# Performance work log

Hardware: AMD Instinct MI355X
Metric: run time of the kernel (lower is better)

Reference implementation:

```python
import jax, jax.numpy as jnp
import numpy as np
import math

HID_DIM = 1024
NUM_HEADS = 8
QK_DIM = HID_DIM // 8  # 128 total, 16 per head


def setup_inputs() -> dict:
    key = jax.random.key(0)
    ks = jax.random.split(key, 7)
    B, M, C = 4, 2048, HID_DIM
    gain = math.sqrt(2.0)  # calculate_gain('relu')

    def xavier(k, fan_in, fan_out):
        std = gain * math.sqrt(2.0 / (fan_in + fan_out))
        a = math.sqrt(3.0) * std
        return jax.random.uniform(k, (fan_out, fan_in), jnp.float32, -a, a)

    x = jax.random.normal(ks[0], (B, M, C), jnp.float32)
    Wq = xavier(ks[1], C, QK_DIM)   # [out, in] like torch Linear
    Wk = xavier(ks[2], C, QK_DIM)
    Wv = xavier(ks[3], C, C)
    bq = jnp.zeros((QK_DIM,), jnp.float32)
    bk = jnp.zeros((QK_DIM,), jnp.float32)
    bv = jnp.zeros((C,), jnp.float32)
    gamma = jnp.zeros((1,), jnp.float32)
    return {"x": x, "Wq": Wq, "bq": bq, "Wk": Wk, "bk": bk,
            "Wv": Wv, "bv": bv, "gamma": gamma}


def reference(x, Wq, bq, Wk, bk, Wv, bv, gamma):
    B, M, C = x.shape
    H = NUM_HEADS
    dqk = QK_DIM // H   # per-head qk dim = 16
    dv = C // H         # per-head v dim = 128
    q = (x @ Wq.T + bq).reshape(B, M, H, dqk)  # [B,M,H,dqk]
    k = (x @ Wk.T + bk).reshape(B, M, H, dqk)
    v = (x @ Wv.T + bv).reshape(B, M, H, dv)
    scores = jnp.einsum('bmhd,bnhd->bhmn', q, k) / math.sqrt(dqk)
    scores = jnp.where(scores >= 0, scores, 0.2 * scores)  # LeakyReLU(0.2)
    beta = jax.nn.softmax(scores, axis=-1)                 # [B,H,M,M]
    out = jnp.einsum('bhmn,bnhd->bmhd', beta, v).reshape(B, M, C)
    return gamma * out + x
```

## Files before the change

### kernel.cpp

```cpp
#include <hip/hip_runtime.h>
#include <hip/hip_bf16.h>

typedef __bf16 bf16_t;
typedef __bf16 bf16x8 __attribute__((ext_vector_type(8)));
typedef float f32x4 __attribute__((ext_vector_type(4)));
typedef float f32x16 __attribute__((ext_vector_type(16)));

#define MTOT 8192
#define CDIM 1024
#define HEADS 8
#define DV 128
#define QKD 128
#define SEQ 2048
#define QSCALE 0.3606737602222409f

struct alignas(8) B4 { bf16_t a, b, c, d; };

__device__ inline bf16x8 cvt8(float4 a, float4 b) {
    bf16x8 v = { (bf16_t)a.x, (bf16_t)a.y, (bf16_t)a.z, (bf16_t)a.w,
                 (bf16_t)b.x, (bf16_t)b.y, (bf16_t)b.z, (bf16_t)b.w };
    return v;
}

__device__ inline void gl_lds16(const bf16_t* g, bf16_t* l) {
    __builtin_amdgcn_global_load_lds(
        (const __attribute__((address_space(1))) void*)g,
        (__attribute__((address_space(3))) void*)l, 16, 0, 0);
}

__device__ inline unsigned cvtpk(float a, float b) {
    unsigned r;
    asm("v_cvt_pk_bf16_f32 %0, %1, %2" : "=v"(r) : "v"(a), "v"(b));
    return r;
}

__device__ inline void plswap(unsigned& a, unsigned& b) {
    asm("v_permlane32_swap_b32 %0, %1" : "+v"(a), "+v"(b));
}

#define XITEMS (MTOT * CDIM / 8)
#define WITEMS (1280 * CDIM / 8)

__global__ __launch_bounds__(256) void cvt_all(
    const float* __restrict__ X,
    const float* __restrict__ Wq, const float* __restrict__ Wk,
    const float* __restrict__ Wv,
    bf16_t* __restrict__ Xb, bf16_t* __restrict__ Wb)
{
    int i = blockIdx.x * blockDim.x + threadIdx.x;
    if (i < XITEMS) {
        const float4* s = reinterpret_cast<const float4*>(X) + (size_t)i * 2;
        reinterpret_cast<bf16x8*>(Xb)[i] = cvt8(s[0], s[1]);
    } else {
        int j = i - XITEMS;
        const float* src;
        if (j < 16384)       src = Wq + (size_t)j * 8;
        else if (j < 32768)  src = Wk + (size_t)(j - 16384) * 8;
        else                 src = Wv + (size_t)(j - 32768) * 8;
        const float4* s = reinterpret_cast<const float4*>(src);
        reinterpret_cast<bf16x8*>(Wb)[j] = cvt8(s[0], s[1]);
    }
}

__global__ __launch_bounds__(256) void qkv_gemm3(
    const bf16_t* __restrict__ Xb, const bf16_t* __restrict__ Wb,
    const float* __restrict__ bq, const float* __restrict__ bk,
    const float* __restrict__ bv,
    bf16_t* __restrict__ Qw, bf16_t* __restrict__ Kw, bf16_t* __restrict__ Vt)
{
    __shared__ bf16_t As[128][64];
    __shared__ bf16_t Bs[128][64];

    const int tid = threadIdx.x;
    const int w = tid >> 6, l = tid & 63;
    const int c = l & 15, q = l >> 4;
    const int rw = w & 1, cw = w >> 1;
    const int bx = blockIdx.x;
    const int m0 = blockIdx.y * 128;

    const bf16_t* Arow = Xb + (size_t)(m0 + w * 8 + (l >> 3)) * CDIM + (l & 7) * 8;
    const bf16_t* Brow = Wb + (size_t)(bx * 128 + w * 8 + (l >> 3)) * CDIM + (l & 7) * 8;

    f32x4 acc[16] = {};

    for (int k0 = 0; k0 < CDIM; k0 += 64) {
        __syncthreads();
        #pragma unroll
        for (int i = 0; i < 4; ++i) {
            gl_lds16(Arow + k0 + (size_t)i * 32 * CDIM, &As[i * 32 + w * 8][0]);
            gl_lds16(Brow + k0 + (size_t)i * 32 * CDIM, &Bs[i * 32 + w * 8][0]);
        }
        __syncthreads();
        #pragma unroll
        for (int kk = 0; kk < 2; ++kk) {
            bf16x8 af[4], bfr[4];
            #pragma unroll
            for (int mt = 0; mt < 4; ++mt)
                af[mt] = *(const bf16x8*)&As[rw * 64 + mt * 16 + c][kk * 32 + q * 8];
            #pragma unroll
            for (int nt = 0; nt < 4; ++nt)
                bfr[nt] = *(const bf16x8*)&Bs[cw * 64 + nt * 16 + c][kk * 32 + q * 8];
            #pragma unroll
            for (int mt = 0; mt < 4; ++mt)
                #pragma unroll
                for (int nt = 0; nt < 4; ++nt)
                    acc[mt * 4 + nt] = __builtin_amdgcn_mfma_f32_16x16x32_bf16(
                        af[mt], bfr[nt], acc[mt * 4 + nt], 0, 0, 0);
        }
    }

    #pragma unroll
    for (int mt = 0; mt < 4; ++mt)
        #pragma unroll
        for (int nt = 0; nt < 4; ++nt) {
            const int cl = cw * 64 + nt * 16 + c;
            f32x4 a = acc[mt * 4 + nt];
            const int mg = m0 + rw * 64 + mt * 16 + q * 4;
            if (bx == 0) {
                const float bb = bq[cl];
                #pragma unroll
                for (int r = 0; r < 4; ++r)
                    Qw[(size_t)(mg + r) * QKD + cl] = (bf16_t)((a[r] + bb) * QSCALE);
            } else if (bx == 1) {
                const float bb = bk[cl];
                #pragma unroll
                for (int r = 0; r < 4; ++r)
                    Kw[(size_t)(mg + r) * QKD + cl] = (bf16_t)(a[r] + bb);
            } else {
                const int h = bx - 2;
                const float bb = bv[h * DV + cl];
                const int bidx = mg >> 11, ml = mg & 2047;
                B4 v{ (bf16_t)(a[0] + bb), (bf16_t)(a[1] + bb),
                      (bf16_t)(a[2] + bb), (bf16_t)(a[3] + bb) };
                *(B4*)(Vt + ((size_t)(bidx * HEADS + h) * DV + cl) * SEQ + ml) = v;
            }
        }
}

__global__ __launch_bounds__(256, 2) void qkv_gemm2(
    const float* __restrict__ X,
    const float* __restrict__ Wq, const float* __restrict__ bq,
    const float* __restrict__ Wk, const float* __restrict__ bk,
    const float* __restrict__ Wv, const float* __restrict__ bv,
    bf16_t* __restrict__ Qw, bf16_t* __restrict__ Kw, bf16_t* __restrict__ Vt)
{
    __shared__ alignas(16) bf16_t As[128][72];
    __shared__ alignas(16) bf16_t Bs[128][72];

    const int tid  = threadIdx.x;
    const int lane = tid & 63, wave = tid >> 6;
    const int c = lane & 15, q = lane >> 4;
    const int rw = wave & 1, cw = wave >> 1;
    const int m0 = blockIdx.y * 128;
    const int nt_idx = blockIdx.x;

    const float* W; const float* bias;
    if (nt_idx == 0)      { W = Wq; bias = bq; }
    else if (nt_idx == 1) { W = Wk; bias = bk; }
    else { W = Wv + (size_t)(nt_idx - 2) * DV * CDIM; bias = bv + (nt_idx - 2) * DV; }

    const int srow = tid >> 1, sseg = tid & 1;
    const int swr = (srow >> 3) & 3;
    const float* ax = X + (size_t)(m0 + srow) * CDIM + sseg * 32;
    const float* bxp = W + (size_t)srow * CDIM + sseg * 32;

    f32x4 acc[16] = {};

    for (int k0 = 0; k0 < CDIM; k0 += 64) {
        __syncthreads();
        #pragma unroll
        for (int i = 0; i < 4; ++i) {
            const int ph = (sseg * 4 + i) ^ swr;
            *(bf16x8*)&As[srow][ph * 8] = cvt8(*(const float4*)(ax + k0 + i * 8),
                                               *(const float4*)(ax + k0 + i * 8 + 4));
            *(bf16x8*)&Bs[srow][ph * 8] = cvt8(*(const float4*)(bxp + k0 + i * 8),
                                               *(const float4*)(bxp + k0 + i * 8 + 4));
        }
        __syncthreads();
        #pragma unroll
        for (int kk = 0; kk < 2; ++kk) {
            bf16x8 af[4], bfr[4];
            #pragma unroll
            for (int mt = 0; mt < 4; ++mt) {
                const int row = rw * 64 + mt * 16 + c;
                af[mt] = *(const bf16x8*)&As[row][((kk * 4 + q) ^ ((row >> 3) & 3)) * 8];
            }
            #pragma unroll
            for (int nt = 0; nt < 4; ++nt) {
                const int row = cw * 64 + nt * 16 + c;
                bfr[nt] = *(const bf16x8*)&Bs[row][((kk * 4 + q) ^ ((row >> 3) & 3)) * 8];
            }
            #pragma unroll
            for (int mt = 0; mt < 4; ++mt)
                #pragma unroll
                for (int nt = 0; nt < 4; ++nt)
                    acc[mt * 4 + nt] = __builtin_amdgcn_mfma_f32_16x16x32_bf16(
                        af[mt], bfr[nt], acc[mt * 4 + nt], 0, 0, 0);
        }
    }

    #pragma unroll
    for (int mt = 0; mt < 4; ++mt)
        #pragma unroll
        for (int nt = 0; nt < 4; ++nt) {
            const int col = cw * 64 + nt * 16 + c;
            const float bb = bias[col];
            f32x4 a = acc[mt * 4 + nt];
            const int mg = m0 + rw * 64 + mt * 16 + q * 4;
            if (nt_idx == 0) {
                #pragma unroll
                for (int r = 0; r < 4; ++r)
                    Qw[(size_t)(mg + r) * QKD + col] = (bf16_t)((a[r] + bb) * QSCALE);
            } else if (nt_idx == 1) {
                #pragma unroll
                for (int r = 0; r < 4; ++r)
                    Kw[(size_t)(mg + r) * QKD + col] = (bf16_t)(a[r] + bb);
            } else {
                const int h = nt_idx - 2;
                const int bidx = mg >> 11, ml = mg & 2047;
                B4 v{ (bf16_t)(a[0] + bb), (bf16_t)(a[1] + bb),
                      (bf16_t)(a[2] + bb), (bf16_t)(a[3] + bb) };
                *(B4*)(Vt + ((size_t)(bidx * HEADS + h) * DV + col) * SEQ + ml) = v;
            }
        }
}

__global__ __launch_bounds__(256, 2) void attn3(
    const bf16_t* __restrict__ Q, const bf16_t* __restrict__ K,
    const bf16_t* __restrict__ Vt, const float* __restrict__ X,
    const float* __restrict__ gptr, float* __restrict__ out)
{
    __shared__ alignas(16) bf16_t Vs[2][128][68];

    const int tid  = threadIdx.x;
    const int lane = tid & 63;
    const int c5 = lane & 31, q1 = lane >> 5;

    const int lin = blockIdx.x + (SEQ / 128) * blockIdx.y;
    const int xcd = lin & 7, jj = lin >> 3;
    const int bh = xcd * 4 + (jj >> 4);
    const int qt = jj & 15;
    const int b = bh >> 3, h = bh & 7;
    const int wave = tid >> 6;
    const int mbase = qt * 128 + wave * 32;

    const bf16x8 qf = *(const bf16x8*)(
        Q + (size_t)(b * SEQ + mbase + c5) * QKD + h * 16 + q1 * 8);

    const bf16x8 ones = { (bf16_t)1.0f, (bf16_t)1.0f, (bf16_t)1.0f, (bf16_t)1.0f,
                          (bf16_t)1.0f, (bf16_t)1.0f, (bf16_t)1.0f, (bf16_t)1.0f };

    f32x16 o[4] = {};
    f32x16 oli = {};

    const bf16_t* Vhead = Vt + (size_t)(b * HEADS + h) * DV * SEQ;
    const bf16_t* Kbase = K + (size_t)(b * SEQ) * QKD + h * 16;

    const int sdv = tid >> 1, sseg = tid & 1;
    const int swv = (sdv >> 3) & 7;

    bf16x8 vA[4], vB[4], kA[2], kB[2];

    union U8 { bf16x8 v; unsigned u[4]; unsigned long long q[2]; };

    #define VS_WR(buf, row, ph, val) do {                                    \
        U8 _u; _u.v = (val);                                                 \
        *(unsigned long long*)&Vs[buf][row][(ph) * 8]     = _u.q[0];         \
        *(unsigned long long*)&Vs[buf][row][(ph) * 8 + 4] = _u.q[1];         \
    } while (0)

    {
        const bf16_t* s0 = Vhead + (size_t)sdv * SEQ + sseg * 32;
        #pragma unroll
        for (int i = 0; i < 4; ++i) vA[i] = *(const bf16x8*)(s0 + i * 8);
        const bf16_t* s1 = s0 + 64;
        #pragma unroll
        for (int i = 0; i < 4; ++i) vB[i] = *(const bf16x8*)(s1 + i * 8);
        #pragma unroll
        for (int blk = 0; blk < 2; ++blk) {
            kA[blk] = *(const bf16x8*)(Kbase + (size_t)(blk * 32 + c5) * QKD + q1 * 8);
            kB[blk] = *(const bf16x8*)(Kbase + (size_t)(64 + blk * 32 + c5) * QKD + q1 * 8);
        }
        #pragma unroll
        for (int i = 0; i < 4; ++i) {
            const int ph = (sseg * 4 + i) ^ swv;
            VS_WR(0, sdv, ph, vA[i]);
        }
        const bf16_t* s2 = s0 + 128;
        #pragma unroll
        for (int i = 0; i < 4; ++i) vA[i] = *(const bf16x8*)(s2 + i * 8);
    }

    #pragma unroll 1
    for (int t = 0; t < 32; t += 2) {
        #pragma unroll
        for (int half = 0; half < 2; ++half) {
            asm volatile("s_waitcnt lgkmcnt(0)" ::: "memory");
            __builtin_amdgcn_s_barrier();
            __builtin_amdgcn_sched_barrier(0);

            #pragma unroll
            for (int i = 0; i < 4; ++i) {
                const int ph = (sseg * 4 + i) ^ swv;
                if (half) { VS_WR(0, sdv, ph, vA[i]); }
                else      { VS_WR(1, sdv, ph, vB[i]); }
            }
            const int cur = t + half;
            const bf16x8 k0f = half ? kB[0] : kA[0];
            const bf16x8 k1f = half ? kB[1] : kA[1];
            {
                const int vt  = (cur + 3 < 32) ? cur + 3 : 31;
                const int kt2 = (cur + 2 < 32) ? cur + 2 : 31;
                const bf16_t* src = Vhead + (size_t)sdv * SEQ + vt * 64 + sseg * 32;
                #pragma unroll
                for (int i = 0; i < 4; ++i) {
                    bf16x8 vv = *(const bf16x8*)(src + i * 8);
                    if (half) vA[i] = vv; else vB[i] = vv;
                }
                #pragma unroll
                for (int blk = 0; blk < 2; ++blk) {
                    bf16x8 kk = *(const bf16x8*)(
                        Kbase + (size_t)(kt2 * 64 + blk * 32 + c5) * QKD + q1 * 8);
                    if (half) kB[blk] = kk; else kA[blk] = kk;
                }
            }

            U8 frag[4];
            #pragma unroll
            for (int blk = 0; blk < 2; ++blk) {
                f32x16 z = {};
                f32x16 s = __builtin_amdgcn_mfma_f32_32x32x16_bf16(
                    blk ? k1f : k0f, qf, z, 0, 0, 0);
                float e[16];
                #pragma unroll
                for (int r = 0; r < 16; ++r) {
                    const float sv = s[r];
                    e[r] = __builtin_amdgcn_exp2f(fmaxf(sv, 0.2f * sv));
                }
                unsigned w0 = cvtpk(e[0], e[1]),   w1 = cvtpk(e[2], e[3]);
                unsigned w2 = cvtpk(e[4], e[5]),   w3 = cvtpk(e[6], e[7]);
                unsigned w4 = cvtpk(e[8], e[9]),   w5 = cvtpk(e[10], e[11]);
                unsigned w6 = cvtpk(e[12], e[13]), w7 = cvtpk(e[14], e[15]);
                plswap(w0, w2); plswap(w1, w3);
                plswap(w4, w6); plswap(w5, w7);
                frag[blk * 2 + 0].u[0] = w0; frag[blk * 2 + 0].u[1] = w1;
                frag[blk * 2 + 0].u[2] = w2; frag[blk * 2 + 0].u[3] = w3;
                frag[blk * 2 + 1].u[0] = w4; frag[blk * 2 + 1].u[1] = w5;
                frag[blk * 2 + 1].u[2] = w6; frag[blk * 2 + 1].u[3] = w7;
            }

            __builtin_amdgcn_s_setprio(1);
            #pragma unroll
            for (int kt = 0; kt < 4; ++kt) {
                const bf16x8 pa = frag[kt].v;
                #pragma unroll
                for (int dvt = 0; dvt < 4; ++dvt) {
                    const int dv = dvt * 32 + c5;
                    const int phB = (kt * 2 + q1) ^ ((dv >> 3) & 7);
                    U8 ur;
                    ur.q[0] = *(const unsigned long long*)&Vs[half][dv][phB * 8];
                    ur.q[1] = *(const unsigned long long*)&Vs[half][dv][phB * 8 + 4];
                    o[dvt] = __builtin_amdgcn_mfma_f32_32x32x16_bf16(
                        pa, ur.v, o[dvt], 0, 0, 0);
                }
                oli = __builtin_amdgcn_mfma_f32_32x32x16_bf16(pa, ones, oli, 0, 0, 0);
            }
            __builtin_amdgcn_s_setprio(0);
        }
    }

    const float g = gptr[0];

    #pragma unroll
    for (int r = 0; r < 16; ++r) {
        const int row = (r & 3) + 8 * (r >> 2) + 4 * q1;
        const float inv = 1.f / oli[r];
        #pragma unroll
        for (int dvt = 0; dvt < 4; ++dvt) {
            const size_t idx = (size_t)(b * SEQ + mbase + row) * CDIM
                             + h * DV + dvt * 32 + c5;
            out[idx] = g * (o[dvt][r] * inv) + X[idx];
        }
    }
    #undef VS_WR
}

extern "C" void kernel_launch(void* const* d_in, const int* in_sizes, int n_in,
                              void* d_out, int out_size, void* d_ws, size_t ws_size,
                              hipStream_t stream) {
    const float* X  = (const float*)d_in[0];
    const float* Wq = (const float*)d_in[1];
    const float* bq = (const float*)d_in[2];
    const float* Wk = (const float*)d_in[3];
    const float* bk = (const float*)d_in[4];
    const float* Wv = (const float*)d_in[5];
    const float* bv = (const float*)d_in[6];
    const float* g  = (const float*)d_in[7];
    float* out = (float*)d_out;

    dim3 blk(256);
    const size_t big_elems = (size_t)MTOT * CDIM + 1280 * CDIM
                           + (size_t)MTOT * QKD * 2 + (size_t)MTOT * CDIM;
    const size_t big_ws = big_elems * sizeof(bf16_t);

    if (ws_size >= big_ws) {
        bf16_t* Xb = (bf16_t*)d_ws;
        bf16_t* Wb = Xb + (size_t)MTOT * CDIM;
        bf16_t* Qw = Wb + (size_t)1280 * CDIM;
        bf16_t* Kw = Qw + (size_t)MTOT * QKD;
        bf16_t* Vt = Kw + (size_t)MTOT * QKD;

        hipLaunchKernelGGL(cvt_all, dim3((XITEMS + WITEMS) / 256), blk, 0, stream,
                           X, Wq, Wk, Wv, Xb, Wb);
        hipLaunchKernelGGL(qkv_gemm3, dim3(10, 64), blk, 0, stream,
                           Xb, Wb, bq, bk, bv, Qw, Kw, Vt);
        hipLaunchKernelGGL(attn3, dim3(SEQ / 128, 32), blk, 0, stream,
                           Qw, Kw, Vt, X, g, out);
    } else {
        bf16_t* Qw = (bf16_t*)d_ws;
        bf16_t* Kw = Qw + (size_t)MTOT * QKD;
        bf16_t* Vt = Kw + (size_t)MTOT * QKD;
        hipLaunchKernelGGL(qkv_gemm2, dim3(10, 64), blk, 0, stream,
                           X, Wq, bq, Wk, bk, Wv, bv, Qw, Kw, Vt);
        hipLaunchKernelGGL(attn3, dim3(SEQ / 128, 32), blk, 0, stream,
                           Qw, Kw, Vt, X, g, out);
    }
}
```

Baseline: 209.9 us.

## Software-pipeline QK softmax one tile ahead and replace ones-MFMA row sum with VALU

Restructures the attention inner loop so the QK^T scores and exp for tile t+1 are computed while the PV MFMAs for tile t run. This lets VALU exp work overlap matrix-core work instead of serializing with it. The softmax denominator, previously computed with an extra MFMA against a ones vector, is now accumulated with scalar adds per lane and combined with a cross-lane shuffle at the end. This costs more live registers for the double fragment buffers and sums the denominator from fp32 values rather than the bf16-rounded ones.

```diff
diff --git a/kernel.cpp b/kernel.cpp
--- a/kernel.cpp
+++ b/kernel.cpp
@@ -15,6 +15,7 @@
 #define QSCALE 0.3606737602222409f
 
 struct alignas(8) B4 { bf16_t a, b, c, d; };
+union U8 { bf16x8 v; unsigned u[4]; unsigned long long q[2]; };
 
 __device__ inline bf16x8 cvt8(float4 a, float4 b) {
     bf16x8 v = { (bf16_t)a.x, (bf16_t)a.y, (bf16_t)a.z, (bf16_t)a.w,
@@ -247,11 +248,8 @@
     const bf16x8 qf = *(const bf16x8*)(
         Q + (size_t)(b * SEQ + mbase + c5) * QKD + h * 16 + q1 * 8);
 
-    const bf16x8 ones = { (bf16_t)1.0f, (bf16_t)1.0f, (bf16_t)1.0f, (bf16_t)1.0f,
-                          (bf16_t)1.0f, (bf16_t)1.0f, (bf16_t)1.0f, (bf16_t)1.0f };
-
+    float li = 0.f;
     f32x16 o[4] = {};
-    f32x16 oli = {};
 
     const bf16_t* Vhead = Vt + (size_t)(b * HEADS + h) * DV * SEQ;
     const bf16_t* Kbase = K + (size_t)(b * SEQ) * QKD + h * 16;
@@ -260,8 +258,7 @@
     const int swv = (sdv >> 3) & 7;
 
     bf16x8 vA[4], vB[4], kA[2], kB[2];
-
-    union U8 { bf16x8 v; unsigned u[4]; unsigned long long q[2]; };
+    U8 fragE[4], fragO[4];
 
     #define VS_WR(buf, row, ph, val) do {                                    \
         U8 _u; _u.v = (val);                                                 \
@@ -269,6 +266,70 @@
         *(unsigned long long*)&Vs[buf][row][(ph) * 8 + 4] = _u.q[1];         \
     } while (0)
 
+    #define QKSM(KF0, KF1, FR) do {                                          \
+        f32x16 _z = {};                                                      \
+        f32x16 _sa = __builtin_amdgcn_mfma_f32_32x32x16_bf16(KF0, qf, _z, 0, 0, 0); \
+        f32x16 _sb = __builtin_amdgcn_mfma_f32_32x32x16_bf16(KF1, qf, _z, 0, 0, 0); \
+        float _ea[16], _eb[16];                                              \
+        _Pragma("unroll")                                                    \
+        for (int _r = 0; _r < 16; ++_r) {                                    \
+            const float _v = _sa[_r];                                        \
+            _ea[_r] = __builtin_amdgcn_exp2f(fmaxf(_v, 0.2f * _v));          \
+            const float _w = _sb[_r];                                        \
+            _eb[_r] = __builtin_amdgcn_exp2f(fmaxf(_w, 0.2f * _w));          \
+        }                                                                    \
+        {                                              \
+            const float _q0 = (_ea[0] + _ea[1]) + (_ea[2] + _ea[3]);         \
+            const float _q1 = (_ea[4] + _ea[5]) + (_ea[6] + _ea[7]);         \
+            const float _q2 = (_ea[8] + _ea[9]) + (_ea[10] + _ea[11]);       \
+            const float _q3 = (_ea[12] + _ea[13]) + (_ea[14] + _ea[15]);     \
+            const float _r0 = (_eb[0] + _eb[1]) + (_eb[2] + _eb[3]);         \
+            const float _r1 = (_eb[4] + _eb[5]) + (_eb[6] + _eb[7]);         \
+            const float _r2 = (_eb[8] + _eb[9]) + (_eb[10] + _eb[11]);       \
+            const float _r3 = (_eb[12] + _eb[13]) + (_eb[14] + _eb[15]);     \
+            li += ((_q0 + _q1) + (_q2 + _q3)) + ((_r0 + _r1) + (_r2 + _r3)); \
+        }                                                                    \
+        {                                                                    \
+            unsigned _w0 = cvtpk(_ea[0], _ea[1]),   _w1 = cvtpk(_ea[2], _ea[3]); \
+            unsigned _w2 = cvtpk(_ea[4], _ea[5]),   _w3 = cvtpk(_ea[6], _ea[7]); \
+            unsigned _w4 = cvtpk(_ea[8], _ea[9]),   _w5 = cvtpk(_ea[10], _ea[11]); \
+            unsigned _w6 = cvtpk(_ea[12], _ea[13]), _w7 = cvtpk(_ea[14], _ea[15]); \
+            plswap(_w0, _w2); plswap(_w1, _w3);                              \
+            plswap(_w4, _w6); plswap(_w5, _w7);                              \
+            FR[0].u[0] = _w0; FR[0].u[1] = _w1; FR[0].u[2] = _w2; FR[0].u[3] = _w3; \
+            FR[1].u[0] = _w4; FR[1].u[1] = _w5; FR[1].u[2] = _w6; FR[1].u[3] = _w7; \
+        }                                                                    \
+        {                                                                    \
+            unsigned _w0 = cvtpk(_eb[0], _eb[1]),   _w1 = cvtpk(_eb[2], _eb[3]); \
+            unsigned _w2 = cvtpk(_eb[4], _eb[5]),   _w3 = cvtpk(_eb[6], _eb[7]); \
+            unsigned _w4 = cvtpk(_eb[8], _eb[9]),   _w5 = cvtpk(_eb[10], _eb[11]); \
+            unsigned _w6 = cvtpk(_eb[12], _eb[13]), _w7 = cvtpk(_eb[14], _eb[15]); \
+            plswap(_w0, _w2); plswap(_w1, _w3);                              \
+            plswap(_w4, _w6); plswap(_w5, _w7);                              \
+            FR[2].u[0] = _w0; FR[2].u[1] = _w1; FR[2].u[2] = _w2; FR[2].u[3] = _w3; \
+            FR[3].u[0] = _w4; FR[3].u[1] = _w5; FR[3].u[2] = _w6; FR[3].u[3] = _w7; \
+        }                                                                    \
+    } while (0)
+
+    #define PV(FR, BUF) do {                                                 \
+        __builtin_amdgcn_s_setprio(1);                                       \
+        _Pragma("unroll")                                                    \
+        for (int _kt = 0; _kt < 4; ++_kt) {                                  \
+            const bf16x8 _pa = FR[_kt].v;                                    \
+            _Pragma("unroll")                                                \
+            for (int _dvt = 0; _dvt < 4; ++_dvt) {                           \
+                const int _dv = _dvt * 32 + c5;                              \
+                const int _ph = (_kt * 2 + q1) ^ ((_dv >> 3) & 7);           \
+                U8 _ur;                                                      \
+                _ur.q[0] = *(const unsigned long long*)&Vs[BUF][_dv][_ph * 8];     \
+                _ur.q[1] = *(const unsigned long long*)&Vs[BUF][_dv][_ph * 8 + 4]; \
+                o[_dvt] = __builtin_amdgcn_mfma_f32_32x32x16_bf16(           \
+                    _pa, _ur.v, o[_dvt], 0, 0, 0);                           \
+            }                                                                \
+        }                                                                    \
+        __builtin_amdgcn_s_setprio(0);                                       \
+    } while (0)
+
     {
         const bf16_t* s0 = Vhead + (size_t)sdv * SEQ + sseg * 32;
         #pragma unroll
@@ -289,100 +350,84 @@
         const bf16_t* s2 = s0 + 128;
         #pragma unroll
         for (int i = 0; i < 4; ++i) vA[i] = *(const bf16x8*)(s2 + i * 8);
+        QKSM(kA[0], kA[1], fragE);
     }
 
     #pragma unroll 1
     for (int t = 0; t < 32; t += 2) {
-        #pragma unroll
-        for (int half = 0; half < 2; ++half) {
+        {
             asm volatile("s_waitcnt lgkmcnt(0)" ::: "memory");
             __builtin_amdgcn_s_barrier();
             __builtin_amdgcn_sched_barrier(0);
-
             #pragma unroll
             for (int i = 0; i < 4; ++i) {
                 const int ph = (sseg * 4 + i) ^ swv;
-                if (half) { VS_WR(0, sdv, ph, vA[i]); }
-                else      { VS_WR(1, sdv, ph, vB[i]); }
-            }
-            const int cur = t + half;
-            const bf16x8 k0f = half ? kB[0] : kA[0];
-            const bf16x8 k1f = half ? kB[1] : kA[1];
+                VS_WR(1, sdv, ph, vB[i]);
+            }
             {
-                const int vt  = (cur + 3 < 32) ? cur + 3 : 31;
-                const int kt2 = (cur + 2 < 32) ? cur + 2 : 31;
+                const int vt = (t + 3 < 32) ? t + 3 : 31;
                 const bf16_t* src = Vhead + (size_t)sdv * SEQ + vt * 64 + sseg * 32;
                 #pragma unroll
-                for (int i = 0; i < 4; ++i) {
-                    bf16x8 vv = *(const bf16x8*)(src + i * 8);
-                    if (half) vA[i] = vv; else vB[i] = vv;
-                }
-                #pragma unroll
-                for (int blk = 0; blk < 2; ++blk) {
-                    bf16x8 kk = *(const bf16x8*)(
+                for (int i = 0; i < 4; ++i) vB[i] = *(const bf16x8*)(src + i * 8);
+            }
+            const bf16x8 nk0 = kB[0], nk1 = kB[1];
+            {
+                const int kt2 = (t + 2 < 32) ? t + 2 : 31;
+                #pragma unroll
+                for (int blk = 0; blk < 2; ++blk)
+                    kA[blk] = *(const bf16x8*)(
                         Kbase + (size_t)(kt2 * 64 + blk * 32 + c5) * QKD + q1 * 8);
-                    if (half) kB[blk] = kk; else kA[blk] = kk;
-                }
-            }
-
-            U8 frag[4];
-            #pragma unroll
-            for (int blk = 0; blk < 2; ++blk) {
-                f32x16 z = {};
-                f32x16 s = __builtin_amdgcn_mfma_f32_32x32x16_bf16(
-                    blk ? k1f : k0f, qf, z, 0, 0, 0);
-                float e[16];
-                #pragma unroll
-                for (int r = 0; r < 16; ++r) {
-                    const float sv = s[r];
-                    e[r] = __builtin_amdgcn_exp2f(fmaxf(sv, 0.2f * sv));
-                }
-                unsigned w0 = cvtpk(e[0], e[1]),   w1 = cvtpk(e[2], e[3]);
-                unsigned w2 = cvtpk(e[4], e[5]),   w3 = cvtpk(e[6], e[7]);
-                unsigned w4 = cvtpk(e[8], e[9]),   w5 = cvtpk(e[10], e[11]);
-                unsigned w6 = cvtpk(e[12], e[13]), w7 = cvtpk(e[14], e[15]);
-                plswap(w0, w2); plswap(w1, w3);
-                plswap(w4, w6); plswap(w5, w7);
-                frag[blk * 2 + 0].u[0] = w0; frag[blk * 2 + 0].u[1] = w1;
-                frag[blk * 2 + 0].u[2] = w2; frag[blk * 2 + 0].u[3] = w3;
-                frag[blk * 2 + 1].u[0] = w4; frag[blk * 2 + 1].u[1] = w5;
-                frag[blk * 2 + 1].u[2] = w6; frag[blk * 2 + 1].u[3] = w7;
-            }
-
-            __builtin_amdgcn_s_setprio(1);
-            #pragma unroll
-            for (int kt = 0; kt < 4; ++kt) {
-                const bf16x8 pa = frag[kt].v;
-                #pragma unroll
-                for (int dvt = 0; dvt < 4; ++dvt) {
-                    const int dv = dvt * 32 + c5;
-                    const int phB = (kt * 2 + q1) ^ ((dv >> 3) & 7);
-                    U8 ur;
-                    ur.q[0] = *(const unsigned long long*)&Vs[half][dv][phB * 8];
-                    ur.q[1] = *(const unsigned long long*)&Vs[half][dv][phB * 8 + 4];
-                    o[dvt] = __builtin_amdgcn_mfma_f32_32x32x16_bf16(
-                        pa, ur.v, o[dvt], 0, 0, 0);
-                }
-                oli = __builtin_amdgcn_mfma_f32_32x32x16_bf16(pa, ones, oli, 0, 0, 0);
-            }
-            __builtin_amdgcn_s_setprio(0);
-        }
-    }
-
+            }
+            QKSM(nk0, nk1, fragO);
+            PV(fragE, 0);
+        }
+        {
+            asm volatile("s_waitcnt lgkmcnt(0)" ::: "memory");
+            __builtin_amdgcn_s_barrier();
+            __builtin_amdgcn_sched_barrier(0);
+            #pragma unroll
+            for (int i = 0; i < 4; ++i) {
+                const int ph = (sseg * 4 + i) ^ swv;
+                VS_WR(0, sdv, ph, vA[i]);
+            }
+            {
+                const int vt = (t + 4 < 32) ? t + 4 : 31;
+                const bf16_t* src = Vhead + (size_t)sdv * SEQ + vt * 64 + sseg * 32;
+                #pragma unroll
+                for (int i = 0; i < 4; ++i) vA[i] = *(const bf16x8*)(src + i * 8);
+            }
+            const bf16x8 nk0 = kA[0], nk1 = kA[1];
+            {
+                const int kt2 = (t + 3 < 32) ? t + 3 : 31;
+                #pragma unroll
+                for (int blk = 0; blk < 2; ++blk)
+                    kB[blk] = *(const bf16x8*)(
+                        Kbase + (size_t)(kt2 * 64 + blk * 32 + c5) * QKD + q1 * 8);
+            }
+            if (t < 30) {
+                QKSM(nk0, nk1, fragE);
+            }
+            PV(fragO, 1);
+        }
+    }
+
+    li += __shfl_xor(li, 32);
+    const float inv = 1.f / li;
     const float g = gptr[0];
 
     #pragma unroll
-    for (int r = 0; r < 16; ++r) {
-        const int row = (r & 3) + 8 * (r >> 2) + 4 * q1;
-        const float inv = 1.f / oli[r];
-        #pragma unroll
-        for (int dvt = 0; dvt < 4; ++dvt) {
+    for (int dvt = 0; dvt < 4; ++dvt)
+        #pragma unroll
+        for (int r = 0; r < 16; ++r) {
+            const int row = (r & 3) + 8 * (r >> 2) + 4 * q1;
+            const float linv = __shfl(inv, row);
             const size_t idx = (size_t)(b * SEQ + mbase + row) * CDIM
                              + h * DV + dvt * 32 + c5;
-            out[idx] = g * (o[dvt][r] * inv) + X[idx];
-        }
-    }
+            out[idx] = g * (o[dvt][r] * linv) + X[idx];
+        }
     #undef VS_WR
+    #undef QKSM
+    #undef PV
 }
 
 extern "C" void kernel_launch(void* const* d_in, const int* in_sizes, int n_in,
```

Result: no change. 210.6 us (+0.3%).
